# Kernel optimization log

Measured on AMD Instinct MI355X. Metric: run time of the kernel, lower is better.

The kernel has to match this reference:

```python
import jax, jax.numpy as jnp
import numpy as np

B = 4096
D = 1024
N = 100000
KS = (10000, 20000, 50000)


def _l2norm(x):
    # F.normalize(p=2, dim=1, eps=1e-12): x / max(||x||, eps)
    n = jnp.sqrt(jnp.sum(x * x, axis=1, keepdims=True))
    return x / jnp.maximum(n, 1e-12)


def setup_inputs() -> dict:
    key = jax.random.key(0)
    ks = jax.random.split(key, 16)
    inp = {}
    inp["anchor"] = jax.random.normal(ks[0], (B, D), jnp.float32)
    inp["index"] = jax.random.randint(ks[1], (B,), 0, N)
    for i, K in enumerate(KS):
        inp[f"inst2cluster{i}"] = jax.random.randint(ks[2 + i], (N,), 0, K)
        inp[f"centroids{i}"] = jax.random.normal(ks[5 + i], (K, D), jnp.float32)
        # density acts as a per-column temperature; keep it bounded away from 0
        inp[f"density{i}"] = jax.random.uniform(ks[8 + i], (K,), jnp.float32, 0.1, 1.0)
    return inp


def reference(anchor, centroids0, centroids1, centroids2,
              density0, density1, density2,
              index, inst2cluster0, inst2cluster1, inst2cluster2):
    Bn = anchor.shape[0]
    a = _l2norm(anchor)
    rows = jnp.arange(Bn)
    cols = jnp.arange(Bn - 1)
    # negatives[i, j] = sim[i, j + (j >= i)] -> row i without its diagonal entry
    neg_idx = cols[None, :] + (cols[None, :] >= rows[:, None])  # [B, B-1]

    scales = [(inst2cluster0, centroids0, density0),
              (inst2cluster1, centroids1, density1),
              (inst2cluster2, centroids2, density2)]
    n_scales = len(scales)

    loss = jnp.zeros(Bn, anchor.dtype)
    for i2c, cent, dens in scales:
        protos = _l2norm(cent)
        pos_id = i2c[index]                       # [B]
        sim = a @ protos[pos_id].T                # [B, B]
        pos = jnp.diagonal(sim)[:, None]          # [B, 1]
        neg = jnp.take_along_axis(sim, neg_idx, axis=1)  # [B, B-1]
        # torch broadcast: [B, B] / [B] divides column j by temp_proto[j]
        logits = jnp.concatenate([pos, neg], axis=1) / dens[pos_id][None, :]
        # CE with label 0, reduction='none'
        ce = jax.nn.logsumexp(logits, axis=1) - logits[:, 0]
        # faithful to the original: division by len(cluster_result) INSIDE the loop
        loss = (loss + ce) / n_scales
    return loss
```

## Files before the change

### kernel.cpp

```cpp
#include <hip/hip_runtime.h>

#define BB 4096
#define DD 1024

typedef float f32x4 __attribute__((ext_vector_type(4)));
typedef short bf16x8 __attribute__((ext_vector_type(8)));

__device__ __forceinline__ unsigned short f2bf(float f) {
  unsigned u = __float_as_uint(f);
  unsigned r = u + 0x7fffu + ((u >> 16) & 1u);
  return (unsigned short)(r >> 16);
}

__device__ __forceinline__ void async16(const void* g, void* l) {
  __builtin_amdgcn_global_load_lds(
      (const __attribute__((address_space(1))) void*)g,
      (__attribute__((address_space(3))) void*)l,
      16, 0, 0);
}

__global__ __launch_bounds__(256) void norm_anchor(const float* __restrict__ x,
                                                   unsigned short* __restrict__ y) {
  __shared__ float sred[4];
  const int row = blockIdx.x;
  const int tid = threadIdx.x;
  const float4 v = ((const float4*)(x + (size_t)row * DD))[tid];
  float ss = v.x * v.x + v.y * v.y + v.z * v.z + v.w * v.w;
#pragma unroll
  for (int off = 32; off > 0; off >>= 1) ss += __shfl_xor(ss, off, 64);
  if ((tid & 63) == 0) sred[tid >> 6] = ss;
  __syncthreads();
  const float tot = sred[0] + sred[1] + sred[2] + sred[3];
  const float inv = 1.0f / fmaxf(sqrtf(tot), 1e-12f);
  ushort4 o;
  o.x = f2bf(v.x * inv);
  o.y = f2bf(v.y * inv);
  o.z = f2bf(v.z * inv);
  o.w = f2bf(v.w * inv);
  ((ushort4*)(y + (size_t)row * DD))[tid] = o;
}

__global__ __launch_bounds__(256) void gather_norm(
    const int* __restrict__ index,
    const int* __restrict__ i2c0, const int* __restrict__ i2c1, const int* __restrict__ i2c2,
    const float* __restrict__ c0, const float* __restrict__ c1, const float* __restrict__ c2,
    const float* __restrict__ d0, const float* __restrict__ d1, const float* __restrict__ d2,
    unsigned short* __restrict__ p16, float* __restrict__ rt) {
  __shared__ float sred[4];
  const int j = blockIdx.x;
  const int s = blockIdx.y;
  const int tid = threadIdx.x;
  const int* i2c = (s == 0) ? i2c0 : (s == 1) ? i2c1 : i2c2;
  const float* cent = (s == 0) ? c0 : (s == 1) ? c1 : c2;
  const float* dens = (s == 0) ? d0 : (s == 1) ? d1 : d2;
  const int pid = i2c[index[j]];
  const float4 v = ((const float4*)(cent + (size_t)pid * DD))[tid];
  float ss = v.x * v.x + v.y * v.y + v.z * v.z + v.w * v.w;
#pragma unroll
  for (int off = 32; off > 0; off >>= 1) ss += __shfl_xor(ss, off, 64);
  if ((tid & 63) == 0) sred[tid >> 6] = ss;
  __syncthreads();
  const float tot = sred[0] + sred[1] + sred[2] + sred[3];
  const float inv = 1.0f / fmaxf(sqrtf(tot), 1e-12f);
  unsigned short* out = p16 + ((size_t)s * BB + j) * DD;
  ushort4 o;
  o.x = f2bf(v.x * inv);
  o.y = f2bf(v.y * inv);
  o.z = f2bf(v.z * inv);
  o.w = f2bf(v.w * inv);
  ((ushort4*)out)[tid] = o;
  if (tid == 0) rt[s * BB + j] = 1.0f / dens[pid];
}

__global__ __launch_bounds__(256) void gemm_nt_bf16(const unsigned short* __restrict__ A,
                                                    const unsigned short* __restrict__ Bm,
                                                    float* __restrict__ C) {
  __shared__ __align__(16) unsigned short lA[128 * 32];
  __shared__ __align__(16) unsigned short lB[128 * 32];
  const int tid = threadIdx.x;
  const int lane = tid & 63;
  const int wave = tid >> 6;
  const int m0 = blockIdx.y * 128;
  const int n0 = blockIdx.x * 128;

  f32x4 acc[4][4];
#pragma unroll
  for (int mi = 0; mi < 4; ++mi)
#pragma unroll
    for (int ni = 0; ni < 4; ++ni) acc[mi][ni] = (f32x4){0.f, 0.f, 0.f, 0.f};

  const int srow = lane >> 2;
  const int scol = (lane & 3) * 8;

  const int wm = (wave >> 1) * 64;
  const int wn = (wave & 1) * 64;
  const int fr = lane & 15;
  const int fk = (lane >> 4) * 8;

  for (int k0 = 0; k0 < DD; k0 += 32) {
#pragma unroll
    for (int c = 0; c < 2; ++c) {
      const int chunk = wave * 2 + c;
      const int r = chunk * 16 + srow;
      const unsigned short* ga = A + (size_t)(m0 + r) * DD + k0 + scol;
      const unsigned short* gb = Bm + (size_t)(n0 + r) * DD + k0 + scol;
      async16(ga, &lA[chunk * 512]);
      async16(gb, &lB[chunk * 512]);
    }
    __syncthreads();

    bf16x8 af[4], bf[4];
#pragma unroll
    for (int mi = 0; mi < 4; ++mi)
      af[mi] = *(const bf16x8*)&lA[(wm + mi * 16 + fr) * 32 + fk];
#pragma unroll
    for (int ni = 0; ni < 4; ++ni)
      bf[ni] = *(const bf16x8*)&lB[(wn + ni * 16 + fr) * 32 + fk];
#pragma unroll
    for (int mi = 0; mi < 4; ++mi)
#pragma unroll
      for (int ni = 0; ni < 4; ++ni)
        acc[mi][ni] = __builtin_amdgcn_mfma_f32_16x16x32_bf16(af[mi], bf[ni], acc[mi][ni], 0, 0, 0);
    __syncthreads();
  }

  const int cm = (lane >> 4) * 4;
#pragma unroll
  for (int mi = 0; mi < 4; ++mi)
#pragma unroll
    for (int ni = 0; ni < 4; ++ni) {
      const int col = n0 + wn + ni * 16 + fr;
#pragma unroll
      for (int r = 0; r < 4; ++r) {
        const int rowi = m0 + wm + mi * 16 + cm + r;
        C[(size_t)rowi * BB + col] = acc[mi][ni][r];
      }
    }
}

__global__ __launch_bounds__(256) void ce_kernel(const float* __restrict__ sim,
                                                 const float* __restrict__ rt,
                                                 float* __restrict__ ce) {
  __shared__ float slog[BB];
  __shared__ float sred[8];
  const int i = blockIdx.x;
  const int tid = threadIdx.x;
  const int lane = tid & 63;
  const int wave = tid >> 6;
  const float* row = sim + (size_t)i * BB;
  const float r0 = rt[0];
  float lmax = -3.4e38f;
  for (int c = tid; c < BB; c += 256) {
    const float v = row[c];
    const float rr = (c == i) ? r0 : ((c < i) ? rt[c + 1] : rt[c]);
    const float l = v * rr;
    slog[c] = l;
    lmax = fmaxf(lmax, l);
  }
#pragma unroll
  for (int off = 32; off > 0; off >>= 1) lmax = fmaxf(lmax, __shfl_xor(lmax, off, 64));
  if (lane == 0) sred[wave] = lmax;
  __syncthreads();
  const float m = fmaxf(fmaxf(sred[0], sred[1]), fmaxf(sred[2], sred[3]));
  float sum = 0.f;
  for (int c = tid; c < BB; c += 256) sum += __expf(slog[c] - m);
#pragma unroll
  for (int off = 32; off > 0; off >>= 1) sum += __shfl_xor(sum, off, 64);
  if (lane == 0) sred[4 + wave] = sum;
  __syncthreads();
  if (tid == 0) {
    const float tot = sred[4] + sred[5] + sred[6] + sred[7];
    ce[i] = m + logf(tot) - slog[i];
  }
}

__global__ __launch_bounds__(256) void combine(const float* __restrict__ ce,
                                               float* __restrict__ out) {
  const int i = blockIdx.x * 256 + threadIdx.x;
  out[i] = ce[i] * (1.0f / 27.0f) + ce[BB + i] * (1.0f / 9.0f) + ce[2 * BB + i] * (1.0f / 3.0f);
}

extern "C" void kernel_launch(void* const* d_in, const int* in_sizes, int n_in,
                              void* d_out, int out_size, void* d_ws, size_t ws_size,
                              hipStream_t stream) {
  const float* anchor = (const float*)d_in[0];
  const int* index    = (const int*)d_in[1];
  const int* i2c0     = (const int*)d_in[2];
  const float* c0     = (const float*)d_in[3];
  const float* de0    = (const float*)d_in[4];
  const int* i2c1     = (const int*)d_in[5];
  const float* c1     = (const float*)d_in[6];
  const float* de1    = (const float*)d_in[7];
  const int* i2c2     = (const int*)d_in[8];
  const float* c2     = (const float*)d_in[9];
  const float* de2    = (const float*)d_in[10];

  char* ws = (char*)d_ws;
  const size_t A16_OFF = 0;
  const size_t P16_OFF = A16_OFF + (size_t)BB * DD * 2;
  const size_t RT_OFF  = P16_OFF + (size_t)3 * BB * DD * 2;
  const size_t CE_OFF  = RT_OFF + (size_t)3 * BB * 4;
  const size_t SIM_OFF = CE_OFF + (size_t)3 * BB * 4;

  unsigned short* a16 = (unsigned short*)(ws + A16_OFF);
  unsigned short* p16 = (unsigned short*)(ws + P16_OFF);
  float* rt  = (float*)(ws + RT_OFF);
  float* cebuf = (float*)(ws + CE_OFF);
  float* sim = (float*)(ws + SIM_OFF);
  float* out = (float*)d_out;

  norm_anchor<<<BB, 256, 0, stream>>>(anchor, a16);
  gather_norm<<<dim3(BB, 3), 256, 0, stream>>>(index, i2c0, i2c1, i2c2,
                                               c0, c1, c2, de0, de1, de2, p16, rt);
  for (int s = 0; s < 3; ++s) {
    gemm_nt_bf16<<<dim3(BB / 128, BB / 128), 256, 0, stream>>>(
        a16, p16 + (size_t)s * BB * DD, sim);
    ce_kernel<<<BB, 256, 0, stream>>>(sim, rt + (size_t)s * BB, cebuf + (size_t)s * BB);
  }
  combine<<<BB / 256, 256, 0, stream>>>(cebuf, out);
}
```

Measured before the change: 537.7 us.

## Fuse GEMM with softmax partial sums via atomics, batch three scales in one launch

Folds the cross-entropy work into the GEMM epilogue. Each tile scales its logits by the per-column temperature, exponentiates them without subtracting a max, reduces per row within the tile, and atomically adds the row sums to a global accumulator. The diagonal logit is written out separately, and the three scales run as one 3D grid. This removes the 64MB similarity-matrix write and read per scale and cuts the kernel launches. In exchange it drops the max-subtraction stabilisation, which relies on bounded logits (cosine similarity divided by a density of at least 0.1) so that exp does not overflow.

```diff
diff --git a/kernel.cpp b/kernel.cpp
--- a/kernel.cpp
+++ b/kernel.cpp
@@ -2,6 +2,7 @@
 
 #define BB 4096
 #define DD 1024
+#define RTS (BB + 16)
 
 typedef float f32x4 __attribute__((ext_vector_type(4)));
 typedef short bf16x8 __attribute__((ext_vector_type(8)));
@@ -45,7 +46,8 @@
     const int* __restrict__ i2c0, const int* __restrict__ i2c1, const int* __restrict__ i2c2,
     const float* __restrict__ c0, const float* __restrict__ c1, const float* __restrict__ c2,
     const float* __restrict__ d0, const float* __restrict__ d1, const float* __restrict__ d2,
-    unsigned short* __restrict__ p16, float* __restrict__ rt) {
+    unsigned short* __restrict__ p16, float* __restrict__ rt,
+    float* __restrict__ rowacc) {
   __shared__ float sred[4];
   const int j = blockIdx.x;
   const int s = blockIdx.y;
@@ -69,19 +71,26 @@
   o.z = f2bf(v.z * inv);
   o.w = f2bf(v.w * inv);
   ((ushort4*)out)[tid] = o;
-  if (tid == 0) rt[s * BB + j] = 1.0f / dens[pid];
-}
-
-__global__ __launch_bounds__(256) void gemm_nt_bf16(const unsigned short* __restrict__ A,
-                                                    const unsigned short* __restrict__ Bm,
-                                                    float* __restrict__ C) {
+  if (tid == 0) rt[(size_t)s * RTS + j] = 1.0f / dens[pid];
+  if (tid == 1) rowacc[(size_t)s * BB + j] = 0.0f;
+}
+
+__global__ __launch_bounds__(256) void gemm_ce_fused(const unsigned short* __restrict__ A,
+                                                     const unsigned short* __restrict__ P,
+                                                     const float* __restrict__ rt,
+                                                     float* __restrict__ rowacc,
+                                                     float* __restrict__ diag) {
   __shared__ __align__(16) unsigned short lA[128 * 32];
   __shared__ __align__(16) unsigned short lB[128 * 32];
+  __shared__ float rowsum[2][128];
   const int tid = threadIdx.x;
   const int lane = tid & 63;
   const int wave = tid >> 6;
   const int m0 = blockIdx.y * 128;
   const int n0 = blockIdx.x * 128;
+  const int s = blockIdx.z;
+  const unsigned short* Bm = P + (size_t)s * BB * DD;
+  const float* rt_s = rt + (size_t)s * RTS;
 
   f32x4 acc[4][4];
 #pragma unroll
@@ -109,75 +118,63 @@
     }
     __syncthreads();
 
-    bf16x8 af[4], bf[4];
+    bf16x8 af[4], bfr[4];
 #pragma unroll
     for (int mi = 0; mi < 4; ++mi)
       af[mi] = *(const bf16x8*)&lA[(wm + mi * 16 + fr) * 32 + fk];
 #pragma unroll
     for (int ni = 0; ni < 4; ++ni)
-      bf[ni] = *(const bf16x8*)&lB[(wn + ni * 16 + fr) * 32 + fk];
+      bfr[ni] = *(const bf16x8*)&lB[(wn + ni * 16 + fr) * 32 + fk];
 #pragma unroll
     for (int mi = 0; mi < 4; ++mi)
 #pragma unroll
       for (int ni = 0; ni < 4; ++ni)
-        acc[mi][ni] = __builtin_amdgcn_mfma_f32_16x16x32_bf16(af[mi], bf[ni], acc[mi][ni], 0, 0, 0);
+        acc[mi][ni] = __builtin_amdgcn_mfma_f32_16x16x32_bf16(af[mi], bfr[ni], acc[mi][ni], 0, 0, 0);
     __syncthreads();
   }
 
   const int cm = (lane >> 4) * 4;
-#pragma unroll
-  for (int mi = 0; mi < 4; ++mi)
-#pragma unroll
-    for (int ni = 0; ni < 4; ++ni) {
-      const int col = n0 + wn + ni * 16 + fr;
-#pragma unroll
-      for (int r = 0; r < 4; ++r) {
-        const int rowi = m0 + wm + mi * 16 + cm + r;
-        C[(size_t)rowi * BB + col] = acc[mi][ni][r];
+  const float rt0 = rt_s[0];
+  float rtc[4], rtp[4];
+#pragma unroll
+  for (int ni = 0; ni < 4; ++ni) {
+    const int col = n0 + wn + ni * 16 + fr;
+    rtc[ni] = rt_s[col];
+    rtp[ni] = rt_s[col + 1];
+  }
+#pragma unroll
+  for (int mi = 0; mi < 4; ++mi) {
+#pragma unroll
+    for (int r = 0; r < 4; ++r) {
+      const int rowi = m0 + wm + mi * 16 + cm + r;
+      float esum = 0.f;
+#pragma unroll
+      for (int ni = 0; ni < 4; ++ni) {
+        const int col = n0 + wn + ni * 16 + fr;
+        const float v = acc[mi][ni][r];
+        const float rr = (col == rowi) ? rt0 : ((col < rowi) ? rtp[ni] : rtc[ni]);
+        const float l = v * rr;
+        if (col == rowi) diag[(size_t)s * BB + rowi] = l;
+        esum += __expf(l);
       }
+#pragma unroll
+      for (int off = 1; off < 16; off <<= 1) esum += __shfl_xor(esum, off, 64);
+      if (fr == 0) rowsum[wave & 1][wm + mi * 16 + cm + r] = esum;
     }
-}
-
-__global__ __launch_bounds__(256) void ce_kernel(const float* __restrict__ sim,
-                                                 const float* __restrict__ rt,
-                                                 float* __restrict__ ce) {
-  __shared__ float slog[BB];
-  __shared__ float sred[8];
-  const int i = blockIdx.x;
-  const int tid = threadIdx.x;
-  const int lane = tid & 63;
-  const int wave = tid >> 6;
-  const float* row = sim + (size_t)i * BB;
-  const float r0 = rt[0];
-  float lmax = -3.4e38f;
-  for (int c = tid; c < BB; c += 256) {
-    const float v = row[c];
-    const float rr = (c == i) ? r0 : ((c < i) ? rt[c + 1] : rt[c]);
-    const float l = v * rr;
-    slog[c] = l;
-    lmax = fmaxf(lmax, l);
   }
-#pragma unroll
-  for (int off = 32; off > 0; off >>= 1) lmax = fmaxf(lmax, __shfl_xor(lmax, off, 64));
-  if (lane == 0) sred[wave] = lmax;
   __syncthreads();
-  const float m = fmaxf(fmaxf(sred[0], sred[1]), fmaxf(sred[2], sred[3]));
-  float sum = 0.f;
-  for (int c = tid; c < BB; c += 256) sum += __expf(slog[c] - m);
-#pragma unroll
-  for (int off = 32; off > 0; off >>= 1) sum += __shfl_xor(sum, off, 64);
-  if (lane == 0) sred[4 + wave] = sum;
-  __syncthreads();
-  if (tid == 0) {
-    const float tot = sred[4] + sred[5] + sred[6] + sred[7];
-    ce[i] = m + logf(tot) - slog[i];
-  }
-}
-
-__global__ __launch_bounds__(256) void combine(const float* __restrict__ ce,
-                                               float* __restrict__ out) {
+  for (int t = tid; t < 128; t += 256)
+    atomicAdd(&rowacc[(size_t)s * BB + m0 + t], rowsum[0][t] + rowsum[1][t]);
+}
+
+__global__ __launch_bounds__(256) void finish(const float* __restrict__ rowacc,
+                                              const float* __restrict__ diag,
+                                              float* __restrict__ out) {
   const int i = blockIdx.x * 256 + threadIdx.x;
-  out[i] = ce[i] * (1.0f / 27.0f) + ce[BB + i] * (1.0f / 9.0f) + ce[2 * BB + i] * (1.0f / 3.0f);
+  const float ce0 = logf(rowacc[i]) - diag[i];
+  const float ce1 = logf(rowacc[BB + i]) - diag[BB + i];
+  const float ce2 = logf(rowacc[2 * BB + i]) - diag[2 * BB + i];
+  out[i] = ce0 * (1.0f / 27.0f) + ce1 * (1.0f / 9.0f) + ce2 * (1.0f / 3.0f);
 }
 
 extern "C" void kernel_launch(void* const* d_in, const int* in_sizes, int n_in,
@@ -199,23 +196,19 @@
   const size_t A16_OFF = 0;
   const size_t P16_OFF = A16_OFF + (size_t)BB * DD * 2;
   const size_t RT_OFF  = P16_OFF + (size_t)3 * BB * DD * 2;
-  const size_t CE_OFF  = RT_OFF + (size_t)3 * BB * 4;
-  const size_t SIM_OFF = CE_OFF + (size_t)3 * BB * 4;
+  const size_t ACC_OFF = RT_OFF + (size_t)3 * RTS * 4;
+  const size_t DIA_OFF = ACC_OFF + (size_t)3 * BB * 4;
 
   unsigned short* a16 = (unsigned short*)(ws + A16_OFF);
   unsigned short* p16 = (unsigned short*)(ws + P16_OFF);
-  float* rt  = (float*)(ws + RT_OFF);
-  float* cebuf = (float*)(ws + CE_OFF);
-  float* sim = (float*)(ws + SIM_OFF);
+  float* rt     = (float*)(ws + RT_OFF);
+  float* rowacc = (float*)(ws + ACC_OFF);
+  float* diag   = (float*)(ws + DIA_OFF);
   float* out = (float*)d_out;
 
   norm_anchor<<<BB, 256, 0, stream>>>(anchor, a16);
   gather_norm<<<dim3(BB, 3), 256, 0, stream>>>(index, i2c0, i2c1, i2c2,
-                                               c0, c1, c2, de0, de1, de2, p16, rt);
-  for (int s = 0; s < 3; ++s) {
-    gemm_nt_bf16<<<dim3(BB / 128, BB / 128), 256, 0, stream>>>(
-        a16, p16 + (size_t)s * BB * DD, sim);
-    ce_kernel<<<BB, 256, 0, stream>>>(sim, rt + (size_t)s * BB, cebuf + (size_t)s * BB);
-  }
-  combine<<<BB / 256, 256, 0, stream>>>(cebuf, out);
-}
+                                               c0, c1, c2, de0, de1, de2, p16, rt, rowacc);
+  gemm_ce_fused<<<dim3(BB / 128, BB / 128, 3), 256, 0, stream>>>(a16, p16, rt, rowacc, diag);
+  finish<<<BB / 256, 256, 0, stream>>>(rowacc, diag, out);
+}
```

After: 441.3 us. -17.9%, faster.
